# Kernel tuning notes

Measured on AMD Instinct MI355X. Metric: run time of the kernel, lower is better.

## Reference

```python
import jax, jax.numpy as jnp
import numpy as np

VOCAB, EMB, HID, TAG, T = 500000, 50, 50, 5, 4096  # HID = hidden_dim//2 per direction
START, STOP, NEG = 3, 4, -10000.0


def setup_inputs() -> dict:
    key = jax.random.key(0)
    ks = jax.random.split(key, 14)
    sentence = jax.random.randint(ks[0], (T,), 0, VOCAB, dtype=jnp.int32)
    embed = jax.random.normal(ks[1], (VOCAB, EMB), dtype=jnp.float32)
    # PyTorch LSTM params, gate order (i, f, g, o); b = b_ih + b_hh fused (same math)
    Wih_f = jax.random.normal(ks[2], (4 * HID, EMB), dtype=jnp.float32) * 0.1
    Whh_f = jax.random.normal(ks[3], (4 * HID, HID), dtype=jnp.float32) * 0.1
    b_f = jax.random.normal(ks[4], (4 * HID,), dtype=jnp.float32) * 0.1
    Wih_b = jax.random.normal(ks[5], (4 * HID, EMB), dtype=jnp.float32) * 0.1
    Whh_b = jax.random.normal(ks[6], (4 * HID, HID), dtype=jnp.float32) * 0.1
    b_b = jax.random.normal(ks[7], (4 * HID,), dtype=jnp.float32) * 0.1
    Wt = jax.random.normal(ks[8], (TAG, 2 * HID), dtype=jnp.float32) * 0.1
    bt = jax.random.normal(ks[9], (TAG,), dtype=jnp.float32) * 0.1
    transitions = jax.random.normal(ks[10], (TAG, TAG), dtype=jnp.float32)
    transitions = transitions.at[START, :].set(NEG).at[:, STOP].set(NEG)
    h0 = jax.random.normal(ks[11], (2, HID), dtype=jnp.float32)  # [fwd/bwd dir]
    c0 = jax.random.normal(ks[12], (2, HID), dtype=jnp.float32)
    return dict(sentence=sentence, embed=embed, Wih_f=Wih_f, Whh_f=Whh_f, b_f=b_f,
                Wih_b=Wih_b, Whh_b=Whh_b, b_b=b_b, Wt=Wt, bt=bt,
                transitions=transitions, h0=h0, c0=c0)


def _lstm_dir(x, h0, c0, Wih, Whh, b):
    # x: [T, EMB] -> hs: [T, HID]; PyTorch gate order i,f,g,o
    def step(carry, xt):
        h, c = carry
        z = xt @ Wih.T + h @ Whh.T + b  # [4H]
        i, f, g, o = jnp.split(z, 4)
        i, f, o = jax.nn.sigmoid(i), jax.nn.sigmoid(f), jax.nn.sigmoid(o)
        c = f * c + i * jnp.tanh(g)
        h = o * jnp.tanh(c)
        return (h, c), h
    _, hs = jax.lax.scan(step, (h0, c0), x)
    return hs


def _lstm_feats(sentence, embed, Wih_f, Whh_f, b_f, Wih_b, Whh_b, b_b, Wt, bt, h0, c0):
    x = embed[sentence]                       # [T, EMB]
    hf = _lstm_dir(x, h0[0], c0[0], Wih_f, Whh_f, b_f)            # [T, HID]
    hb = _lstm_dir(x[::-1], h0[1], c0[1], Wih_b, Whh_b, b_b)[::-1]  # [T, HID]
    h = jnp.concatenate([hf, hb], axis=-1)    # [T, 2*HID]
    return h @ Wt.T + bt                       # [T, TAG]


def reference(sentence, embed, Wih_f, Whh_f, b_f, Wih_b, Whh_b, b_b, Wt, bt, transitions, h0, c0):
    feats = _lstm_feats(sentence, embed, Wih_f, Whh_f, b_f, Wih_b, Whh_b, b_b, Wt, bt, h0, c0)

    fv0 = jnp.full((TAG,), NEG, dtype=feats.dtype).at[START].set(0.0)

    def vstep(fv, feat):
        m = fv[None, :] + transitions          # [next_tag, prev_tag]
        bp = jnp.argmax(m, axis=1)             # [TAG] best prev for each next
        fv_new = jnp.max(m, axis=1) + feat
        return fv_new, bp

    fv, bps = jax.lax.scan(vstep, fv0, feats)  # bps: [T, TAG]
    terminal = fv + transitions[STOP]
    last = jnp.argmax(terminal)

    def bt_step(tag, bp):
        return bp[tag], tag                    # carry prev tag, emit current tag

    _start, path = jax.lax.scan(bt_step, last, bps, reverse=True)
    score = terminal[last]
    return path.astype(jnp.int32), score
```

## Files before the change

### kernel.cpp

```cpp
#include <hip/hip_runtime.h>
#include <math.h>

#define EMB 50
#define HID 50
#define G4  200
#define NTAG 5
#define NEGV (-10000.0f)
#define TAG_START 3
#define TAG_STOP  4
#define T_MAX 4096
#define TB 8
#define WPAD 52

typedef float f32x4 __attribute__((ext_vector_type(4)));
typedef float f32x2 __attribute__((ext_vector_type(2)));

#define LO2(v) __builtin_shufflevector(v, v, 0, 1)
#define HI2(v) __builtin_shufflevector(v, v, 2, 3)

__global__ __launch_bounds__(256)
void k_embed_proj(const int* __restrict__ sent,
                  const float* __restrict__ embed,
                  const float* __restrict__ Wf, const float* __restrict__ bf,
                  const float* __restrict__ Wb, const float* __restrict__ bb,
                  float* __restrict__ pre, int T) {
  __shared__ __align__(16) float Wl[G4 * WPAD];
  __shared__ __align__(16) float xl[TB * WPAD];
  const int tid = threadIdx.x;
  const int t0  = blockIdx.x * TB;
  int ntt = T - t0; if (ntt > TB) ntt = TB;

  for (int e = tid; e < ntt * EMB; e += 256) {
    int tt = e / EMB, k = e - tt * EMB;
    xl[tt * WPAD + k] = embed[(long long)sent[t0 + tt] * EMB + k];
  }

  for (int ph = 0; ph < 2; ++ph) {
    const float* W = ph ? Wb : Wf;
    const float* b = ph ? bb : bf;
    __syncthreads();
    for (int e = tid; e < G4 * EMB; e += 256) {
      int r = e / EMB, k = e - r * EMB;
      Wl[r * WPAD + k] = W[e];
    }
    __syncthreads();
    float* outBase = pre + ((long long)ph * (T + 4) + 2) * G4;
    for (int o = tid; o < ntt * G4; o += 256) {
      int tt = o / G4, j = o - tt * G4;
      const float* wr_ = &Wl[j * WPAD];
      const float* xx  = &xl[tt * WPAD];
      f32x2 a2 = {0.f, 0.f};
#pragma unroll
      for (int k4 = 0; k4 < 12; ++k4) {
        f32x4 wv = *(const f32x4*)&wr_[4 * k4];
        f32x4 xv = *(const f32x4*)&xx[4 * k4];
        a2 += LO2(wv) * LO2(xv);
        a2 += HI2(wv) * HI2(xv);
      }
      a2.x += wr_[48] * xx[48];
      a2.y += wr_[49] * xx[49];
      float acc = b[j] + a2.x + a2.y;
      int unit = j % HID, gate = j / HID;
      outBase[(long long)(t0 + tt) * G4 + unit * 4 + gate] = acc;
    }
  }
}

#define DPP_XOR1(v) __int_as_float(__builtin_amdgcn_update_dpp(0, __float_as_int(v), 0xB1, 0xF, 0xF, true))
#define DPP_XOR2(v) __int_as_float(__builtin_amdgcn_update_dpp(0, __float_as_int(v), 0x4E, 0xF, 0xF, true))

__device__ __forceinline__ float dot16(f32x4 w0, f32x4 w1, f32x4 w2, f32x4 w3,
                                       f32x4 x0, f32x4 x1, f32x4 x2, f32x4 x3) {
  f32x2 a = {0.f, 0.f}, b = {0.f, 0.f};
  a += LO2(w0) * LO2(x0);  b += HI2(w0) * HI2(x0);
  a += LO2(w1) * LO2(x1);  b += HI2(w1) * HI2(x1);
  a += LO2(w2) * LO2(x2);  b += HI2(w2) * HI2(x2);
  a += LO2(w3) * LO2(x3);  b += HI2(w3) * HI2(x3);
  return (a.x + b.x) + (a.y + b.y);
}

#define LSTM_STEP(HRbuf, HWbuf)                                              \
  {                                                                          \
    const float* HR = HRbuf;                                                 \
    float*       HW = HWbuf;                                                 \
    f32x4 mp = *(const f32x4*)pp;                                            \
    pp += sG4;                                                               \
    f32x4 x0 = *(const f32x4*)&HR[16 * q + 0];                               \
    f32x4 x1 = *(const f32x4*)&HR[16 * q + 4];                               \
    f32x4 x2 = *(const f32x4*)&HR[16 * q + 8];                               \
    f32x4 x3 = *(const f32x4*)&HR[16 * q + 12];                              \
    float pi = dot16(Wi0, Wi1, Wi2, Wi3, x0, x1, x2, x3);                    \
    float pf = dot16(Wf0, Wf1, Wf2, Wf3, x0, x1, x2, x3);                    \
    float pg = dot16(Wg0, Wg1, Wg2, Wg3, x0, x1, x2, x3);                    \
    float po = dot16(Wo0, Wo1, Wo2, Wo3, x0, x1, x2, x3);                    \
    pi += DPP_XOR1(pi); pi += DPP_XOR2(pi);                                  \
    pf += DPP_XOR1(pf); pf += DPP_XOR2(pf);                                  \
    pg += DPP_XOR1(pg); pg += DPP_XOR2(pg);                                  \
    po += DPP_XOR1(po); po += DPP_XOR2(po);                                  \
    float zi = cp.x + pi, zf = cp.y + pf, zg = cp.z + pg, zo = cp.w + po;    \
    float ei = __expf(-zi), ef2 = __expf(-zf);                               \
    float eg2 = __expf(-zg), eo2 = __expf(-zo);                              \
    float si = __builtin_amdgcn_rcpf(1.f + ei);                              \
    float sf = __builtin_amdgcn_rcpf(1.f + ef2);                             \
    float so = __builtin_amdgcn_rcpf(1.f + eo2);                             \
    float tg = 2.f * __builtin_amdgcn_rcpf(1.f + eg2 * eg2) - 1.f;           \
    c = sf * c + si * tg;                                                    \
    float e2 = __expf(-2.f * c);                                             \
    float tc = 2.f * __builtin_amdgcn_rcpf(1.f + e2) - 1.f;                  \
    float h = so * tc;                                                       \
    if (wr) {                                                                \
      HW[jq] = h;                                                            \
      *hsp = h;                                                              \
    }                                                                        \
    asm volatile("s_waitcnt lgkmcnt(0)\n\ts_barrier" ::: "memory");          \
    hsp += sH;                                                               \
    cp = np; np = mp;                                                        \
  }

__global__ __launch_bounds__(256)
__attribute__((amdgpu_waves_per_eu(1, 1)))
void k_lstm(const float* __restrict__ pre,
            const float* __restrict__ Whh_f,
            const float* __restrict__ Whh_b,
            const float* __restrict__ h0, const float* __restrict__ c0,
            float* __restrict__ hs, int T) {
  const int d   = blockIdx.x;
  const int tid = threadIdx.x;
  const int j   = tid >> 2;
  const int q   = tid & 3;
  const int jq  = (j < HID) ? j : 0;
  const bool wr = (q == 0) && (j < HID);
  const float* __restrict__ Whh  = d ? Whh_b : Whh_f;
  const float* __restrict__ preD = pre + ((long long)d * (T + 4) + 2) * G4;

  __shared__ __align__(16) float hA[64];
  __shared__ __align__(16) float hB[64];

  const float* p0 = Whh + (long long)(0 * HID + jq) * HID + 16 * q;
  const float* p1 = Whh + (long long)(1 * HID + jq) * HID + 16 * q;
  const float* p2 = Whh + (long long)(2 * HID + jq) * HID + 16 * q;
  const float* p3 = Whh + (long long)(3 * HID + jq) * HID + 16 * q;
  f32x4 Wi0, Wi1, Wi2, Wi3, Wf0, Wf1, Wf2, Wf3;
  f32x4 Wg0, Wg1, Wg2, Wg3, Wo0, Wo1, Wo2, Wo3;
  asm volatile(
      "global_load_dwordx4 %0,  %16, off\n\t"
      "global_load_dwordx4 %1,  %16, off offset:16\n\t"
      "global_load_dwordx4 %2,  %16, off offset:32\n\t"
      "global_load_dwordx4 %3,  %16, off offset:48\n\t"
      "global_load_dwordx4 %4,  %17, off\n\t"
      "global_load_dwordx4 %5,  %17, off offset:16\n\t"
      "global_load_dwordx4 %6,  %17, off offset:32\n\t"
      "global_load_dwordx4 %7,  %17, off offset:48\n\t"
      "global_load_dwordx4 %8,  %18, off\n\t"
      "global_load_dwordx4 %9,  %18, off offset:16\n\t"
      "global_load_dwordx4 %10, %18, off offset:32\n\t"
      "global_load_dwordx4 %11, %18, off offset:48\n\t"
      "global_load_dwordx4 %12, %19, off\n\t"
      "global_load_dwordx4 %13, %19, off offset:16\n\t"
      "global_load_dwordx4 %14, %19, off offset:32\n\t"
      "global_load_dwordx4 %15, %19, off offset:48\n\t"
      "s_waitcnt vmcnt(0)"
      : "=&v"(Wi0), "=&v"(Wi1), "=&v"(Wi2), "=&v"(Wi3),
        "=&v"(Wf0), "=&v"(Wf1), "=&v"(Wf2), "=&v"(Wf3),
        "=&v"(Wg0), "=&v"(Wg1), "=&v"(Wg2), "=&v"(Wg3),
        "=&v"(Wo0), "=&v"(Wo1), "=&v"(Wo2), "=&v"(Wo3)
      : "v"(p0), "v"(p1), "v"(p2), "v"(p3));

  if (q == 3) {
    const f32x4 z4 = {0.f, 0.f, 0.f, 0.f};
    Wi0.z = 0.f; Wi0.w = 0.f; Wi1 = z4; Wi2 = z4; Wi3 = z4;
    Wf0.z = 0.f; Wf0.w = 0.f; Wf1 = z4; Wf2 = z4; Wf3 = z4;
    Wg0.z = 0.f; Wg0.w = 0.f; Wg1 = z4; Wg2 = z4; Wg3 = z4;
    Wo0.z = 0.f; Wo0.w = 0.f; Wo1 = z4; Wo2 = z4; Wo3 = z4;
  }

  float c = c0[d * HID + jq];
  if (tid < 64) { hA[tid] = 0.f; hB[tid] = 0.f; }
  __syncthreads();
  if (wr) hA[jq] = h0[d * HID + jq];
  __syncthreads();

  const int s = d ? -1 : 1;
  const int t0 = d ? (T - 1) : 0;
  const long long sG4 = (long long)s * G4;
  const long long sH  = (long long)s * (2 * HID);

  f32x4 cp = *(const f32x4*)&preD[(long long)t0 * G4 + 4 * jq];
  f32x4 np = *(const f32x4*)&preD[(long long)(t0 + s) * G4 + 4 * jq];
  const float* pp = preD + (long long)(t0 + 2 * s) * G4 + 4 * jq;
  float* hsp = hs + (long long)t0 * (2 * HID) + d * HID + jq;

  for (int it = 0; it < T; it += 2) {
    LSTM_STEP(hA, hB)
    LSTM_STEP(hB, hA)
  }
}

__global__ void k_feats(const float* __restrict__ hs, const float* __restrict__ Wt,
                        const float* __restrict__ bt, float* __restrict__ feats, int T) {
  int g = blockIdx.x * blockDim.x + threadIdx.x;
  if (g >= T * NTAG) return;
  int t = g / NTAG, m = g % NTAG;
  const float* h = hs + (long long)t * (2 * HID);
  const float* w = Wt + m * (2 * HID);
  float a = bt[m];
#pragma unroll
  for (int k = 0; k < 2 * HID; ++k) a += w[k] * h[k];
  feats[g] = a;
}

__global__ __launch_bounds__(64, 1)
void k_vchunk(const float* __restrict__ feats,
              const float* __restrict__ trans,
              float* __restrict__ fvh, float* __restrict__ misc,
              float* __restrict__ out, int T) {
  const int lane = threadIdx.x;
  const int L    = T >> 6;
  const int c0   = lane * L;

  __shared__ float Pl[64][26];

  float tr[NTAG * NTAG];
#pragma unroll
  for (int i = 0; i < NTAG * NTAG; ++i) tr[i] = trans[i];

  float P[25];
  {
    float ft[5];
#pragma unroll
    for (int k = 0; k < 5; ++k) ft[k] = feats[c0 * 5 + k];
#pragma unroll
    for (int n = 0; n < 5; ++n)
#pragma unroll
      for (int p = 0; p < 5; ++p) P[n * 5 + p] = tr[n * 5 + p] + ft[n];
  }
  for (int i = 1; i < L; ++i) {
    int t = c0 + i;
    float ft[5];
#pragma unroll
    for (int k = 0; k < 5; ++k) ft[k] = feats[t * 5 + k];
    float NP[25];
#pragma unroll
    for (int n = 0; n < 5; ++n) {
#pragma unroll
      for (int p = 0; p < 5; ++p) {
        float m = tr[n * 5 + 0] + P[0 + p];
        m = fmaxf(m, tr[n * 5 + 1] + P[5 + p]);
        m = fmaxf(m, tr[n * 5 + 2] + P[10 + p]);
        m = fmaxf(m, tr[n * 5 + 3] + P[15 + p]);
        m = fmaxf(m, tr[n * 5 + 4] + P[20 + p]);
        NP[n * 5 + p] = m + ft[n];
      }
    }
#pragma unroll
    for (int e = 0; e < 25; ++e) P[e] = NP[e];
  }
#pragma unroll
  for (int e = 0; e < 25; ++e) Pl[lane][e] = P[e];
  __syncthreads();

  float v0 = NEGV, v1 = NEGV, v2 = NEGV, v3 = 0.f, v4 = NEGV;
  float s0 = 0.f, s1 = 0.f, s2 = 0.f, s3 = 0.f, s4 = 0.f;
  for (int cc = 0; cc < 64; ++cc) {
    bool mine = (cc == lane);
    s0 = mine ? v0 : s0; s1 = mine ? v1 : s1; s2 = mine ? v2 : s2;
    s3 = mine ? v3 : s3; s4 = mine ? v4 : s4;
    float nv[5];
#pragma unroll
    for (int n = 0; n < 5; ++n) {
      float m = Pl[cc][n * 5 + 0] + v0;
      m = fmaxf(m, Pl[cc][n * 5 + 1] + v1);
      m = fmaxf(m, Pl[cc][n * 5 + 2] + v2);
      m = fmaxf(m, Pl[cc][n * 5 + 3] + v3);
      m = fmaxf(m, Pl[cc][n * 5 + 4] + v4);
      nv[n] = m;
    }
    v0 = nv[0]; v1 = nv[1]; v2 = nv[2]; v3 = nv[3]; v4 = nv[4];
  }

  float f0 = s0, f1 = s1, f2 = s2, f3 = s3, f4 = s4;
  for (int i = 0; i < L; ++i) {
    int t = c0 + i;
    fvh[t * 5 + 0] = f0; fvh[t * 5 + 1] = f1; fvh[t * 5 + 2] = f2;
    fvh[t * 5 + 3] = f3; fvh[t * 5 + 4] = f4;
    float ft0 = feats[t * 5 + 0], ft1 = feats[t * 5 + 1], ft2 = feats[t * 5 + 2];
    float ft3 = feats[t * 5 + 3], ft4 = feats[t * 5 + 4];
    float n0 = fmaxf(fmaxf(fmaxf(f0 + tr[0],  f1 + tr[1]),  fmaxf(f2 + tr[2],  f3 + tr[3])),  f4 + tr[4])  + ft0;
    float n1 = fmaxf(fmaxf(fmaxf(f0 + tr[5],  f1 + tr[6]),  fmaxf(f2 + tr[7],  f3 + tr[8])),  f4 + tr[9])  + ft1;
    float n2 = fmaxf(fmaxf(fmaxf(f0 + tr[10], f1 + tr[11]), fmaxf(f2 + tr[12], f3 + tr[13])), f4 + tr[14]) + ft2;
    float n3 = fmaxf(fmaxf(fmaxf(f0 + tr[15], f1 + tr[16]), fmaxf(f2 + tr[17], f3 + tr[18])), f4 + tr[19]) + ft3;
    float n4 = fmaxf(fmaxf(fmaxf(f0 + tr[20], f1 + tr[21]), fmaxf(f2 + tr[22], f3 + tr[23])), f4 + tr[24]) + ft4;
    f0 = n0; f1 = n1; f2 = n2; f3 = n3; f4 = n4;
  }

  if (lane == 63) {
    float b0 = f0 + tr[TAG_STOP * 5 + 0], b1 = f1 + tr[TAG_STOP * 5 + 1];
    float b2 = f2 + tr[TAG_STOP * 5 + 2], b3 = f3 + tr[TAG_STOP * 5 + 3];
    float b4 = f4 + tr[TAG_STOP * 5 + 4];
    int last = 0; float best = b0;
    if (b1 > best) { best = b1; last = 1; }
    if (b2 > best) { best = b2; last = 2; }
    if (b3 > best) { best = b3; last = 3; }
    if (b4 > best) { best = b4; last = 4; }
    out[T] = best; misc[0] = (float)last;
  }
}

__global__ __launch_bounds__(1024) void k_vbt(const float* __restrict__ trans,
                        const float* __restrict__ fvh, const float* __restrict__ misc,
                        float* __restrict__ out, int T) {
  __shared__ unsigned int bufA[T_MAX];
  __shared__ unsigned int bufB[T_MAX];
  int tid = threadIdx.x;

  {
    float tr[NTAG * NTAG];
#pragma unroll
    for (int i = 0; i < NTAG * NTAG; ++i) tr[i] = trans[i];
    for (int t = tid; t < T; t += 1024) {
      unsigned pack;
      if (t == T - 1) {
        pack = 0u | (1u << 3) | (2u << 6) | (3u << 9) | (4u << 12);
      } else {
        const float* fv = fvh + (long long)(t + 1) * 5;
        float g0 = fv[0], g1 = fv[1], g2 = fv[2], g3 = fv[3], g4 = fv[4];
        pack = 0u;
#pragma unroll
        for (int nx = 0; nx < NTAG; ++nx) {
          float v0 = g0 + tr[nx * 5 + 0], v1 = g1 + tr[nx * 5 + 1], v2 = g2 + tr[nx * 5 + 2];
          float v3 = g3 + tr[nx * 5 + 3], v4 = g4 + tr[nx * 5 + 4];
          int bi = 0; float bv = v0;
          if (v1 > bv) { bv = v1; bi = 1; }
          if (v2 > bv) { bv = v2; bi = 2; }
          if (v3 > bv) { bv = v3; bi = 3; }
          if (v4 > bv) { bv = v4; bi = 4; }
          pack |= (unsigned)bi << (3 * nx);
        }
      }
      bufA[t] = pack;
    }
  }
  __syncthreads();

  unsigned int* cur = bufA;
  unsigned int* nxt = bufB;
  for (int dstep = 1; dstep < T; dstep <<= 1) {
    for (int t = tid; t < T; t += 1024) {
      unsigned v = cur[t];
      int u = t + dstep;
      if (u < T) {
        unsigned qq_ = cur[u];
        unsigned r = 0u;
#pragma unroll
        for (int x = 0; x < NTAG; ++x) {
          unsigned qs = (qq_ >> (3 * x)) & 7u;
          unsigned pp = (v >> (3 * qs)) & 7u;
          r |= pp << (3 * x);
        }
        v = r;
      }
      nxt[t] = v;
    }
    __syncthreads();
    unsigned int* tmp = cur; cur = nxt; nxt = tmp;
  }

  int last = (int)misc[0];
  for (int t = tid; t < T; t += 1024) {
    out[t] = (float)((cur[t] >> (3 * last)) & 7u);
  }
}

extern "C" void kernel_launch(void* const* d_in, const int* in_sizes, int n_in,
                              void* d_out, int out_size, void* d_ws, size_t ws_size,
                              hipStream_t stream) {
  const int*   sent  = (const int*)  d_in[0];
  const float* embed = (const float*)d_in[1];
  const float* Wih_f = (const float*)d_in[2];
  const float* Whh_f = (const float*)d_in[3];
  const float* b_f   = (const float*)d_in[4];
  const float* Wih_b = (const float*)d_in[5];
  const float* Whh_b = (const float*)d_in[6];
  const float* b_b   = (const float*)d_in[7];
  const float* Wt    = (const float*)d_in[8];
  const float* bt    = (const float*)d_in[9];
  const float* trans = (const float*)d_in[10];
  const float* h0    = (const float*)d_in[11];
  const float* c0    = (const float*)d_in[12];
  int T = in_sizes[0];

  float* out = (float*)d_out;
  float* pre   = (float*)d_ws;
  float* hs    = pre + 2 * (size_t)(T + 4) * G4;
  float* feats = hs + (size_t)T * 2 * HID;
  float* fvh   = feats + (size_t)T * NTAG;
  float* misc  = fvh + (size_t)(T + 1) * NTAG;

  k_embed_proj<<<(T + TB - 1) / TB, 256, 0, stream>>>(sent, embed, Wih_f, b_f, Wih_b, b_b, pre, T);
  k_lstm<<<2, 256, 0, stream>>>(pre, Whh_f, Whh_b, h0, c0, hs, T);
  k_feats<<<(T * NTAG + 255) / 256, 256, 0, stream>>>(hs, Wt, bt, feats, T);
  k_vchunk<<<1, 64, 0, stream>>>(feats, trans, fvh, misc, out, T);
  k_vbt<<<1, 1024, 0, stream>>>(trans, fvh, misc, out, T);
}
```

Measured before the change: 1.330 ms.

## Fuse feature projection, Viterbi chunk scan, and backtrace into one kernel

Merges the tag-feature projection, chunked Viterbi forward pass and backtrace kernels into a single 1024-thread block, separated by __syncthreads instead of kernel boundaries. This removes two kernel launches and their inter-kernel gaps. The feature dot products now use float4 loads and paired FMAs. The trade-off is that the projection runs on one workgroup instead of many blocks, and feats/fvh still go through global memory within the same block.

```diff
diff --git a/kernel.cpp b/kernel.cpp
--- a/kernel.cpp
+++ b/kernel.cpp
@@ -196,122 +196,128 @@
   }
 }
 
-__global__ void k_feats(const float* __restrict__ hs, const float* __restrict__ Wt,
-                        const float* __restrict__ bt, float* __restrict__ feats, int T) {
-  int g = blockIdx.x * blockDim.x + threadIdx.x;
-  if (g >= T * NTAG) return;
-  int t = g / NTAG, m = g % NTAG;
-  const float* h = hs + (long long)t * (2 * HID);
-  const float* w = Wt + m * (2 * HID);
-  float a = bt[m];
-#pragma unroll
-  for (int k = 0; k < 2 * HID; ++k) a += w[k] * h[k];
-  feats[g] = a;
-}
-
-__global__ __launch_bounds__(64, 1)
-void k_vchunk(const float* __restrict__ feats,
-              const float* __restrict__ trans,
-              float* __restrict__ fvh, float* __restrict__ misc,
-              float* __restrict__ out, int T) {
-  const int lane = threadIdx.x;
-  const int L    = T >> 6;
-  const int c0   = lane * L;
-
+__global__ __launch_bounds__(1024)
+void k_vfused(const float* __restrict__ hs, const float* __restrict__ Wt,
+              const float* __restrict__ bt, const float* __restrict__ trans,
+              float* __restrict__ feats, float* __restrict__ fvh,
+              float* __restrict__ misc, float* __restrict__ out, int T) {
   __shared__ float Pl[64][26];
-
-  float tr[NTAG * NTAG];
-#pragma unroll
-  for (int i = 0; i < NTAG * NTAG; ++i) tr[i] = trans[i];
-
-  float P[25];
-  {
-    float ft[5];
-#pragma unroll
-    for (int k = 0; k < 5; ++k) ft[k] = feats[c0 * 5 + k];
-#pragma unroll
-    for (int n = 0; n < 5; ++n)
-#pragma unroll
-      for (int p = 0; p < 5; ++p) P[n * 5 + p] = tr[n * 5 + p] + ft[n];
-  }
-  for (int i = 1; i < L; ++i) {
-    int t = c0 + i;
-    float ft[5];
-#pragma unroll
-    for (int k = 0; k < 5; ++k) ft[k] = feats[t * 5 + k];
-    float NP[25];
-#pragma unroll
-    for (int n = 0; n < 5; ++n) {
-#pragma unroll
-      for (int p = 0; p < 5; ++p) {
-        float m = tr[n * 5 + 0] + P[0 + p];
-        m = fmaxf(m, tr[n * 5 + 1] + P[5 + p]);
-        m = fmaxf(m, tr[n * 5 + 2] + P[10 + p]);
-        m = fmaxf(m, tr[n * 5 + 3] + P[15 + p]);
-        m = fmaxf(m, tr[n * 5 + 4] + P[20 + p]);
-        NP[n * 5 + p] = m + ft[n];
-      }
-    }
-#pragma unroll
-    for (int e = 0; e < 25; ++e) P[e] = NP[e];
-  }
-#pragma unroll
-  for (int e = 0; e < 25; ++e) Pl[lane][e] = P[e];
-  __syncthreads();
-
-  float v0 = NEGV, v1 = NEGV, v2 = NEGV, v3 = 0.f, v4 = NEGV;
-  float s0 = 0.f, s1 = 0.f, s2 = 0.f, s3 = 0.f, s4 = 0.f;
-  for (int cc = 0; cc < 64; ++cc) {
-    bool mine = (cc == lane);
-    s0 = mine ? v0 : s0; s1 = mine ? v1 : s1; s2 = mine ? v2 : s2;
-    s3 = mine ? v3 : s3; s4 = mine ? v4 : s4;
-    float nv[5];
-#pragma unroll
-    for (int n = 0; n < 5; ++n) {
-      float m = Pl[cc][n * 5 + 0] + v0;
-      m = fmaxf(m, Pl[cc][n * 5 + 1] + v1);
-      m = fmaxf(m, Pl[cc][n * 5 + 2] + v2);
-      m = fmaxf(m, Pl[cc][n * 5 + 3] + v3);
-      m = fmaxf(m, Pl[cc][n * 5 + 4] + v4);
-      nv[n] = m;
-    }
-    v0 = nv[0]; v1 = nv[1]; v2 = nv[2]; v3 = nv[3]; v4 = nv[4];
-  }
-
-  float f0 = s0, f1 = s1, f2 = s2, f3 = s3, f4 = s4;
-  for (int i = 0; i < L; ++i) {
-    int t = c0 + i;
-    fvh[t * 5 + 0] = f0; fvh[t * 5 + 1] = f1; fvh[t * 5 + 2] = f2;
-    fvh[t * 5 + 3] = f3; fvh[t * 5 + 4] = f4;
-    float ft0 = feats[t * 5 + 0], ft1 = feats[t * 5 + 1], ft2 = feats[t * 5 + 2];
-    float ft3 = feats[t * 5 + 3], ft4 = feats[t * 5 + 4];
-    float n0 = fmaxf(fmaxf(fmaxf(f0 + tr[0],  f1 + tr[1]),  fmaxf(f2 + tr[2],  f3 + tr[3])),  f4 + tr[4])  + ft0;
-    float n1 = fmaxf(fmaxf(fmaxf(f0 + tr[5],  f1 + tr[6]),  fmaxf(f2 + tr[7],  f3 + tr[8])),  f4 + tr[9])  + ft1;
-    float n2 = fmaxf(fmaxf(fmaxf(f0 + tr[10], f1 + tr[11]), fmaxf(f2 + tr[12], f3 + tr[13])), f4 + tr[14]) + ft2;
-    float n3 = fmaxf(fmaxf(fmaxf(f0 + tr[15], f1 + tr[16]), fmaxf(f2 + tr[17], f3 + tr[18])), f4 + tr[19]) + ft3;
-    float n4 = fmaxf(fmaxf(fmaxf(f0 + tr[20], f1 + tr[21]), fmaxf(f2 + tr[22], f3 + tr[23])), f4 + tr[24]) + ft4;
-    f0 = n0; f1 = n1; f2 = n2; f3 = n3; f4 = n4;
-  }
-
-  if (lane == 63) {
-    float b0 = f0 + tr[TAG_STOP * 5 + 0], b1 = f1 + tr[TAG_STOP * 5 + 1];
-    float b2 = f2 + tr[TAG_STOP * 5 + 2], b3 = f3 + tr[TAG_STOP * 5 + 3];
-    float b4 = f4 + tr[TAG_STOP * 5 + 4];
-    int last = 0; float best = b0;
-    if (b1 > best) { best = b1; last = 1; }
-    if (b2 > best) { best = b2; last = 2; }
-    if (b3 > best) { best = b3; last = 3; }
-    if (b4 > best) { best = b4; last = 4; }
-    out[T] = best; misc[0] = (float)last;
-  }
-}
-
-__global__ __launch_bounds__(1024) void k_vbt(const float* __restrict__ trans,
-                        const float* __restrict__ fvh, const float* __restrict__ misc,
-                        float* __restrict__ out, int T) {
   __shared__ unsigned int bufA[T_MAX];
   __shared__ unsigned int bufB[T_MAX];
-  int tid = threadIdx.x;
+  const int tid = threadIdx.x;
+
+  for (int g = tid; g < T * NTAG; g += 1024) {
+    int t = g / NTAG, m = g - t * NTAG;
+    const float* h = hs + (long long)t * (2 * HID);
+    const float* w = Wt + m * (2 * HID);
+    f32x2 a2 = {0.f, 0.f};
+#pragma unroll
+    for (int k4 = 0; k4 < 25; ++k4) {
+      f32x4 hv = *(const f32x4*)&h[4 * k4];
+      f32x4 wv = *(const f32x4*)&w[4 * k4];
+      a2 += LO2(wv) * LO2(hv);
+      a2 += HI2(wv) * HI2(hv);
+    }
+    feats[g] = bt[m] + a2.x + a2.y;
+  }
+  __syncthreads();
+
+  const int L = T >> 6;
+
+  if (tid < 64) {
+    const int c0 = tid * L;
+    float tr[NTAG * NTAG];
+#pragma unroll
+    for (int i = 0; i < NTAG * NTAG; ++i) tr[i] = trans[i];
+    float P[25];
+    {
+      float ft[5];
+#pragma unroll
+      for (int k = 0; k < 5; ++k) ft[k] = feats[c0 * 5 + k];
+#pragma unroll
+      for (int n = 0; n < 5; ++n)
+#pragma unroll
+        for (int p = 0; p < 5; ++p) P[n * 5 + p] = tr[n * 5 + p] + ft[n];
+    }
+    for (int i = 1; i < L; ++i) {
+      int t = c0 + i;
+      float ft[5];
+#pragma unroll
+      for (int k = 0; k < 5; ++k) ft[k] = feats[t * 5 + k];
+      float NP[25];
+#pragma unroll
+      for (int n = 0; n < 5; ++n) {
+#pragma unroll
+        for (int p = 0; p < 5; ++p) {
+          float m = tr[n * 5 + 0] + P[0 + p];
+          m = fmaxf(m, tr[n * 5 + 1] + P[5 + p]);
+          m = fmaxf(m, tr[n * 5 + 2] + P[10 + p]);
+          m = fmaxf(m, tr[n * 5 + 3] + P[15 + p]);
+          m = fmaxf(m, tr[n * 5 + 4] + P[20 + p]);
+          NP[n * 5 + p] = m + ft[n];
+        }
+      }
+#pragma unroll
+      for (int e = 0; e < 25; ++e) P[e] = NP[e];
+    }
+#pragma unroll
+    for (int e = 0; e < 25; ++e) Pl[tid][e] = P[e];
+  }
+  __syncthreads();
+
+  if (tid < 64) {
+    const int c0 = tid * L;
+    float tr[NTAG * NTAG];
+#pragma unroll
+    for (int i = 0; i < NTAG * NTAG; ++i) tr[i] = trans[i];
+
+    float v0 = NEGV, v1 = NEGV, v2 = NEGV, v3 = 0.f, v4 = NEGV;
+    float s0 = 0.f, s1 = 0.f, s2 = 0.f, s3 = 0.f, s4 = 0.f;
+    for (int cc = 0; cc < 64; ++cc) {
+      bool mine = (cc == tid);
+      s0 = mine ? v0 : s0; s1 = mine ? v1 : s1; s2 = mine ? v2 : s2;
+      s3 = mine ? v3 : s3; s4 = mine ? v4 : s4;
+      float nv[5];
+#pragma unroll
+      for (int n = 0; n < 5; ++n) {
+        float m = Pl[cc][n * 5 + 0] + v0;
+        m = fmaxf(m, Pl[cc][n * 5 + 1] + v1);
+        m = fmaxf(m, Pl[cc][n * 5 + 2] + v2);
+        m = fmaxf(m, Pl[cc][n * 5 + 3] + v3);
+        m = fmaxf(m, Pl[cc][n * 5 + 4] + v4);
+        nv[n] = m;
+      }
+      v0 = nv[0]; v1 = nv[1]; v2 = nv[2]; v3 = nv[3]; v4 = nv[4];
+    }
+
+    float f0 = s0, f1 = s1, f2 = s2, f3 = s3, f4 = s4;
+    for (int i = 0; i < L; ++i) {
+      int t = c0 + i;
+      fvh[t * 5 + 0] = f0; fvh[t * 5 + 1] = f1; fvh[t * 5 + 2] = f2;
+      fvh[t * 5 + 3] = f3; fvh[t * 5 + 4] = f4;
+      float ft0 = feats[t * 5 + 0], ft1 = feats[t * 5 + 1], ft2 = feats[t * 5 + 2];
+      float ft3 = feats[t * 5 + 3], ft4 = feats[t * 5 + 4];
+      float n0 = fmaxf(fmaxf(fmaxf(f0 + tr[0],  f1 + tr[1]),  fmaxf(f2 + tr[2],  f3 + tr[3])),  f4 + tr[4])  + ft0;
+      float n1 = fmaxf(fmaxf(fmaxf(f0 + tr[5],  f1 + tr[6]),  fmaxf(f2 + tr[7],  f3 + tr[8])),  f4 + tr[9])  + ft1;
+      float n2 = fmaxf(fmaxf(fmaxf(f0 + tr[10], f1 + tr[11]), fmaxf(f2 + tr[12], f3 + tr[13])), f4 + tr[14]) + ft2;
+      float n3 = fmaxf(fmaxf(fmaxf(f0 + tr[15], f1 + tr[16]), fmaxf(f2 + tr[17], f3 + tr[18])), f4 + tr[19]) + ft3;
+      float n4 = fmaxf(fmaxf(fmaxf(f0 + tr[20], f1 + tr[21]), fmaxf(f2 + tr[22], f3 + tr[23])), f4 + tr[24]) + ft4;
+      f0 = n0; f1 = n1; f2 = n2; f3 = n3; f4 = n4;
+    }
+
+    if (tid == 63) {
+      float b0 = f0 + tr[TAG_STOP * 5 + 0], b1 = f1 + tr[TAG_STOP * 5 + 1];
+      float b2 = f2 + tr[TAG_STOP * 5 + 2], b3 = f3 + tr[TAG_STOP * 5 + 3];
+      float b4 = f4 + tr[TAG_STOP * 5 + 4];
+      int last = 0; float best = b0;
+      if (b1 > best) { best = b1; last = 1; }
+      if (b2 > best) { best = b2; last = 2; }
+      if (b3 > best) { best = b3; last = 3; }
+      if (b4 > best) { best = b4; last = 4; }
+      out[T] = best; misc[0] = (float)last;
+    }
+  }
+  __syncthreads();
 
   {
     float tr[NTAG * NTAG];
@@ -398,7 +404,5 @@
 
   k_embed_proj<<<(T + TB - 1) / TB, 256, 0, stream>>>(sent, embed, Wih_f, b_f, Wih_b, b_b, pre, T);
   k_lstm<<<2, 256, 0, stream>>>(pre, Whh_f, Whh_b, h0, c0, hs, T);
-  k_feats<<<(T * NTAG + 255) / 256, 256, 0, stream>>>(hs, Wt, bt, feats, T);
-  k_vchunk<<<1, 64, 0, stream>>>(feats, trans, fvh, misc, out, T);
-  k_vbt<<<1, 1024, 0, stream>>>(trans, fvh, misc, out, T);
+  k_vfused<<<1, 1024, 0, stream>>>(hs, Wt, bt, trans, feats, fvh, misc, out, T);
 }
```

Result: slower. 1.517 ms (+14.1%).
